# Performance work log

Hardware: AMD Instinct MI355X
Metric: run time of the kernel (lower is better)

Reference implementation:

```python
import jax, jax.numpy as jnp
import numpy as np
import math

HIDDEN = 2048
N_Q = 16
N_KV = 8
HEAD_DIM = 128
THETA = 10000.0
RANK = 8
ALPHA = 16
LORA_SCALING = ALPHA / RANK  # 2.0
SCALING = 1.0 / math.sqrt(HEAD_DIM)


def setup_inputs() -> dict:
    key = jax.random.key(0)
    ks = jax.random.split(key, 14)
    B, S = 2, 2048
    std = 0.02
    inp = {
        "x": jax.random.normal(ks[0], (B, S, HIDDEN), dtype=jnp.float32),
        # nn.Linear weights: [out_features, in_features]
        "Wq": jax.random.normal(ks[1], (N_Q * HEAD_DIM, HIDDEN), dtype=jnp.float32) * std,
        "Wk": jax.random.normal(ks[2], (N_KV * HEAD_DIM, HIDDEN), dtype=jnp.float32) * std,
        "Wv": jax.random.normal(ks[3], (N_KV * HEAD_DIM, HIDDEN), dtype=jnp.float32) * std,
        "Wo": jax.random.normal(ks[4], (HIDDEN, N_Q * HEAD_DIM), dtype=jnp.float32) * std,
        "qA": jax.random.normal(ks[5], (RANK, HIDDEN), dtype=jnp.float32) * std,
        "qB": jax.random.normal(ks[6], (N_Q * HEAD_DIM, RANK), dtype=jnp.float32) * std,
        "kA": jax.random.normal(ks[7], (RANK, HIDDEN), dtype=jnp.float32) * std,
        "kB": jax.random.normal(ks[8], (N_KV * HEAD_DIM, RANK), dtype=jnp.float32) * std,
        "vA": jax.random.normal(ks[9], (RANK, HIDDEN), dtype=jnp.float32) * std,
        "vB": jax.random.normal(ks[10], (N_KV * HEAD_DIM, RANK), dtype=jnp.float32) * std,
        "oA": jax.random.normal(ks[11], (RANK, N_Q * HEAD_DIM), dtype=jnp.float32) * std,
        "oB": jax.random.normal(ks[12], (HIDDEN, RANK), dtype=jnp.float32) * std,
    }
    return inp


def _rope_cos_sin(seq_len, dtype):
    inv_freq = 1.0 / (THETA ** (jnp.arange(0, HEAD_DIM, 2, dtype=jnp.float32) / HEAD_DIM))
    t = jnp.arange(seq_len, dtype=jnp.float32)
    freqs = t[:, None] * inv_freq[None, :]  # [S, D/2]
    return jnp.cos(freqs).astype(dtype), jnp.sin(freqs).astype(dtype)


def _apply_rope(x, cos, sin):
    # x: [B, H, S, D]; interleaved real/imag pairs on last dim
    xr = x[..., ::2]
    xi = x[..., 1::2]
    rr = xr * cos - xi * sin
    ri = xr * sin + xi * cos
    return jnp.stack([rr, ri], axis=-1).reshape(x.shape)


def _forward(x, Wq, Wk, Wv, Wo, qA, qB, kA, kB, vA, vB, oA, oB):
    B, S, H = x.shape
    # base projections + LoRA (low-rank path kept factored: (x @ A^T) @ B^T)
    q = x @ Wq.T + ((x @ qA.T) @ qB.T) * LORA_SCALING  # [B,S,NQ*D]
    k = x @ Wk.T + ((x @ kA.T) @ kB.T) * LORA_SCALING  # [B,S,NKV*D]
    v = x @ Wv.T + ((x @ vA.T) @ vB.T) * LORA_SCALING
    q = q.reshape(B, S, N_Q, HEAD_DIM).transpose(0, 2, 1, 3)   # [B,NQ,S,D]
    k = k.reshape(B, S, N_KV, HEAD_DIM).transpose(0, 2, 1, 3)  # [B,NKV,S,D]
    v = v.reshape(B, S, N_KV, HEAD_DIM).transpose(0, 2, 1, 3)
    cos, sin = _rope_cos_sin(S, x.dtype)  # [S, D/2] each
    q = _apply_rope(q, cos, sin)
    k = _apply_rope(k, cos, sin)
    if N_Q != N_KV:
        rep = N_Q // N_KV
        k = jnp.repeat(k, rep, axis=1)  # [B,NQ,S,D]
        v = jnp.repeat(v, rep, axis=1)
    scores = jnp.einsum('bhqd,bhkd->bhqk', q, k) * SCALING
    causal = jnp.tril(jnp.ones((S, S), dtype=bool))
    scores = jnp.where(causal, scores, -jnp.inf)
    attn = jax.nn.softmax(scores, axis=-1).astype(v.dtype)
    out = jnp.einsum('bhqk,bhkd->bhqd', attn, v)  # [B,NQ,S,D]
    out = out.transpose(0, 2, 1, 3).reshape(B, S, N_Q * HEAD_DIM)
    return out @ Wo.T + ((out @ oA.T) @ oB.T) * LORA_SCALING


def reference(x, Wq, Wk, Wv, Wo, qA, qB, kA, kB, vA, vB, oA, oB):
    return _forward(x, Wq, Wk, Wv, Wo, qA, qB, kA, kB, vA, vB, oA, oB)
```

## Files before the change

kernel.cpp:

```cpp
#include <hip/hip_runtime.h>
#include <hip/hip_bf16.h>
#include <cmath>

#define HIDDEN 2048
#define SEQ 2048
#define BATCH 2
#define NQ 16
#define NKV 8
#define HD 128
#define RANKL 8
#define LORA_SCALE 2.0f
#define INV_SQRT_D 0.08838834764831845f
#define LOG2E 1.4426950408889634f
#define SM_SCALE (INV_SQRT_D * LOG2E)

typedef unsigned short ushort_t;
typedef __bf16 bf16x8 __attribute__((ext_vector_type(8)));
typedef float f32x4 __attribute__((ext_vector_type(4)));

static __device__ __forceinline__ ushort_t f2bf(float f) {
    __hip_bfloat16 h = __float2bfloat16(f);
    return *(ushort_t*)&h;
}
static __device__ __forceinline__ float bf2f(ushort_t u) {
    unsigned int v = ((unsigned int)u) << 16;
    return __builtin_bit_cast(float, v);
}
static __device__ __forceinline__ void gload_lds16(const ushort_t* g, ushort_t* l) {
    __builtin_amdgcn_global_load_lds(
        (const __attribute__((address_space(1))) unsigned int*)g,
        (__attribute__((address_space(3))) unsigned int*)l, 16, 0, 0);
}
static __device__ __forceinline__ bf16x8 pack8(float4 a, float4 b) {
    uint4 u;
    u.x = (unsigned int)f2bf(a.x) | ((unsigned int)f2bf(a.y) << 16);
    u.y = (unsigned int)f2bf(a.z) | ((unsigned int)f2bf(a.w) << 16);
    u.z = (unsigned int)f2bf(b.x) | ((unsigned int)f2bf(b.y) << 16);
    u.w = (unsigned int)f2bf(b.z) | ((unsigned int)f2bf(b.w) << 16);
    return __builtin_bit_cast(bf16x8, u);
}

#define PREP_UNITS 10496
__global__ __launch_bounds__(256) void prep_fused(
    const float* __restrict__ X, ushort_t* __restrict__ Xbf,
    const float* __restrict__ qA, const float* __restrict__ kA,
    const float* __restrict__ vA,
    float* __restrict__ xa_q, float* __restrict__ xa_k,
    float* __restrict__ xa_v,
    const float* __restrict__ Wq, const float* __restrict__ Wk,
    const float* __restrict__ Wv, const float* __restrict__ Wo,
    ushort_t* __restrict__ Wqb, ushort_t* __restrict__ Wkb,
    ushort_t* __restrict__ Wvb, ushort_t* __restrict__ Wob)
{
    __shared__ f32x4 red[4][2][64];
    const int t = threadIdx.x;

    for (int bid = blockIdx.x; bid < PREP_UNITS; bid += gridDim.x) {
        if (bid < 4096) {
            int c0 = t * 8;
            const float* xr = X + (size_t)bid * HIDDEN + c0;
            float4 a = *(const float4*)xr;
            float4 b = *(const float4*)(xr + 4);
            uint4 o;
            o.x = (unsigned int)f2bf(a.x) | ((unsigned int)f2bf(a.y) << 16);
            o.y = (unsigned int)f2bf(a.z) | ((unsigned int)f2bf(a.w) << 16);
            o.z = (unsigned int)f2bf(b.x) | ((unsigned int)f2bf(b.y) << 16);
            o.w = (unsigned int)f2bf(b.z) | ((unsigned int)f2bf(b.w) << 16);
            *(uint4*)(Xbf + (size_t)bid * HIDDEN + c0) = o;
        } else if (bid < 10240) {
            size_t i = (size_t)(bid - 4096) * 256 + t;
            const float* src; ushort_t* dst; size_t j;
            if (i < 524288)       { src = Wq; dst = Wqb; j = i; }
            else if (i < 786432)  { src = Wk; dst = Wkb; j = i - 524288; }
            else if (i < 1048576) { src = Wv; dst = Wvb; j = i - 786432; }
            else                  { src = Wo; dst = Wob; j = i - 1048576; }
            const float4* p = (const float4*)src + j * 2;
            float4 a = p[0], b = p[1];
            uint4 o;
            o.x = (unsigned int)f2bf(a.x) | ((unsigned int)f2bf(a.y) << 16);
            o.y = (unsigned int)f2bf(a.z) | ((unsigned int)f2bf(a.w) << 16);
            o.z = (unsigned int)f2bf(b.x) | ((unsigned int)f2bf(b.y) << 16);
            o.w = (unsigned int)f2bf(b.z) | ((unsigned int)f2bf(b.w) << 16);
            *(uint4*)(dst + j * 8) = o;
        } else {
            const int m0 = (bid - 10240) * 16;
            const int lane = t & 63;
            const int w = t >> 6;
            const int c = lane & 15;
            const int quad = lane >> 4;

            const float* b0 = (c < 8) ? (qA + (size_t)c * HIDDEN)
                                      : (kA + (size_t)(c - 8) * HIDDEN);
            const float* b1 = vA + (size_t)(c & 7) * HIDDEN;
            const bool b1v = (c < 8);
            const float* ax = X + (size_t)(m0 + c) * HIDDEN;

            f32x4 acc0 = (f32x4){0.f, 0.f, 0.f, 0.f};
            f32x4 acc1 = (f32x4){0.f, 0.f, 0.f, 0.f};
            const int kbase = w * 512 + quad * 8;
#pragma unroll
            for (int ks = 0; ks < 16; ++ks) {
                const int k = kbase + ks * 32;
                float4 x0 = *(const float4*)&ax[k];
                float4 x1 = *(const float4*)&ax[k + 4];
                float4 p0a = *(const float4*)&b0[k];
                float4 p0b = *(const float4*)&b0[k + 4];
                float4 p1a = {0.f, 0.f, 0.f, 0.f}, p1b = {0.f, 0.f, 0.f, 0.f};
                if (b1v) { p1a = *(const float4*)&b1[k]; p1b = *(const float4*)&b1[k + 4]; }
                bf16x8 af = pack8(x0, x1);
                bf16x8 bf0 = pack8(p0a, p0b);
                bf16x8 bf1 = pack8(p1a, p1b);
                acc0 = __builtin_amdgcn_mfma_f32_16x16x32_bf16(af, bf0, acc0, 0, 0, 0);
                acc1 = __builtin_amdgcn_mfma_f32_16x16x32_bf16(af, bf1, acc1, 0, 0, 0);
            }
            red[w][0][lane] = acc0;
            red[w][1][lane] = acc1;
            __syncthreads();
            if (t < 64) {
#pragma unroll
                for (int nt = 0; nt < 2; ++nt) {
                    f32x4 s = red[0][nt][t];
#pragma unroll
                    for (int ww = 1; ww < 4; ++ww) {
                        f32x4 o = red[ww][nt][t];
                        s[0] += o[0]; s[1] += o[1]; s[2] += o[2]; s[3] += o[3];
                    }
                    int col = nt * 16 + (t & 15);
                    if (col < 24) {
                        float* dst = (col < 8) ? xa_q : (col < 16) ? xa_k : xa_v;
                        int cc = col & 7;
                        int row0 = m0 + (t >> 4) * 4;
#pragma unroll
                        for (int r = 0; r < 4; ++r)
                            dst[(size_t)(row0 + r) * RANKL + cc] = s[r];
                    }
                }
            }
            __syncthreads();
        }
    }
}

__global__ __launch_bounds__(256) void lora_o_mfma(
    const ushort_t* __restrict__ Xo, const float* __restrict__ oA,
    float* __restrict__ xa_o)
{
    __shared__ f32x4 red[4][64];
    const int t = threadIdx.x;
    const int lane = t & 63;
    const int w = t >> 6;
    const int c = lane & 15;
    const int quad = lane >> 4;
    const int m0 = blockIdx.x * 16;

    const ushort_t* ax = Xo + (size_t)(m0 + c) * (NQ * HD);
    const float* b0 = oA + (size_t)(c & 7) * (NQ * HD);
    const bool bv = (c < 8);

    f32x4 acc = (f32x4){0.f, 0.f, 0.f, 0.f};
    const int kbase = w * 512 + quad * 8;
#pragma unroll
    for (int ks = 0; ks < 16; ++ks) {
        const int k = kbase + ks * 32;
        bf16x8 af = *(const bf16x8*)&ax[k];
        float4 pa = {0.f, 0.f, 0.f, 0.f}, pb = {0.f, 0.f, 0.f, 0.f};
        if (bv) { pa = *(const float4*)&b0[k]; pb = *(const float4*)&b0[k + 4]; }
        bf16x8 bf = pack8(pa, pb);
        acc = __builtin_amdgcn_mfma_f32_16x16x32_bf16(af, bf, acc, 0, 0, 0);
    }
    red[w][lane] = acc;
    __syncthreads();
    if (t < 64) {
        f32x4 s = red[0][t];
#pragma unroll
        for (int ww = 1; ww < 4; ++ww) {
            f32x4 o = red[ww][t];
            s[0] += o[0]; s[1] += o[1]; s[2] += o[2]; s[3] += o[3];
        }
        int col = t & 15;
        if (col < 8) {
            int row0 = m0 + (t >> 4) * 4;
#pragma unroll
            for (int r = 0; r < 4; ++r)
                xa_o[(size_t)(row0 + r) * RANKL + col] = s[r];
        }
    }
}

static __device__ __forceinline__ void gemm_core(
    const ushort_t* __restrict__ A, const ushort_t* __restrict__ B,
    void* __restrict__ Cout, int N, int K, int bm, int bn,
    const float* __restrict__ xa, const float* __restrict__ LB,
    float lscale, int out_bf16, ushort_t* As, ushort_t* Bs)
{
    const int t = threadIdx.x;
    const int lane = t & 63;
    const int w = t >> 6;
    const int quad = lane >> 4;
    const int c = lane & 15;

    const int wm = (w & 1) * 64;
    const int wn = (w >> 1) * 64;

    f32x4 acc[4][4];
#pragma unroll
    for (int i = 0; i < 4; i++)
#pragma unroll
        for (int j = 0; j < 4; j++) acc[i][j] = (f32x4){0.f, 0.f, 0.f, 0.f};

    const int p0 = w * 64 + lane;
    const int p1 = 256 + w * 64 + lane;
    const int r0 = p0 >> 2, g0 = (p0 & 3) ^ ((p0 >> 3) & 3);
    const int r1 = p1 >> 2, g1 = (p1 & 3) ^ ((p1 >> 3) & 3);
    const ushort_t* gA0 = A + (size_t)(bm + r0) * K + g0 * 8;
    const ushort_t* gA1 = A + (size_t)(bm + r1) * K + g1 * 8;
    const ushort_t* gB0 = B + (size_t)(bn + r0) * K + g0 * 8;
    const ushort_t* gB1 = B + (size_t)(bn + r1) * K + g1 * 8;
    ushort_t* lA0 = As + (size_t)(w * 64) * 8;
    ushort_t* lA1 = As + (size_t)(256 + w * 64) * 8;
    ushort_t* lB0 = Bs + (size_t)(w * 64) * 8;
    ushort_t* lB1 = Bs + (size_t)(256 + w * 64) * 8;

    const int csw = quad ^ ((c >> 1) & 3);

    for (int k0 = 0; k0 < K; k0 += 32) {
        __syncthreads();
        gload_lds16(gA0 + k0, lA0);
        gload_lds16(gA1 + k0, lA1);
        gload_lds16(gB0 + k0, lB0);
        gload_lds16(gB1 + k0, lB1);
        __syncthreads();

        bf16x8 af[4], bfr[4];
#pragma unroll
        for (int mt = 0; mt < 4; mt++)
            af[mt] = *(const bf16x8*)&As[((wm + mt * 16 + c) * 4 + csw) * 8];
#pragma unroll
        for (int nt = 0; nt < 4; nt++)
            bfr[nt] = *(const bf16x8*)&Bs[((wn + nt * 16 + c) * 4 + csw) * 8];
#pragma unroll
        for (int mt = 0; mt < 4; mt++)
#pragma unroll
            for (int nt = 0; nt < 4; nt++)
                acc[mt][nt] = __builtin_amdgcn_mfma_f32_16x16x32_bf16(
                    af[mt], bfr[nt], acc[mt][nt], 0, 0, 0);
    }

    float lb[4][RANKL];
#pragma unroll
    for (int nt = 0; nt < 4; nt++) {
        int col = bn + wn + nt * 16 + c;
        float4 u = *(const float4*)&LB[(size_t)col * RANKL];
        float4 v = *(const float4*)&LB[(size_t)col * RANKL + 4];
        lb[nt][0] = u.x; lb[nt][1] = u.y; lb[nt][2] = u.z; lb[nt][3] = u.w;
        lb[nt][4] = v.x; lb[nt][5] = v.y; lb[nt][6] = v.z; lb[nt][7] = v.w;
    }
#pragma unroll
    for (int mt = 0; mt < 4; mt++) {
        float la[4][RANKL];
#pragma unroll
        for (int r = 0; r < 4; r++) {
            int row = bm + wm + mt * 16 + quad * 4 + r;
            float4 u = *(const float4*)&xa[(size_t)row * RANKL];
            float4 v = *(const float4*)&xa[(size_t)row * RANKL + 4];
            la[r][0] = u.x; la[r][1] = u.y; la[r][2] = u.z; la[r][3] = u.w;
            la[r][4] = v.x; la[r][5] = v.y; la[r][6] = v.z; la[r][7] = v.w;
        }
#pragma unroll
        for (int nt = 0; nt < 4; nt++) {
#pragma unroll
            for (int r = 0; r < 4; r++) {
                float s = 0.f;
#pragma unroll
                for (int k = 0; k < RANKL; k++) s += la[r][k] * lb[nt][k];
                float val = acc[mt][nt][r] + lscale * s;
                size_t row = bm + wm + mt * 16 + quad * 4 + r;
                size_t col = bn + wn + nt * 16 + c;
                if (out_bf16)
                    ((ushort_t*)Cout)[row * N + col] = f2bf(val);
                else
                    ((float*)Cout)[row * N + col] = val;
            }
        }
    }
}

#define BKT 64
#define NKT (HIDDEN / BKT)

__global__ __launch_bounds__(512, 2) void gemm_qkv256(
    const ushort_t* __restrict__ A,
    const ushort_t* __restrict__ Wqb, const ushort_t* __restrict__ Wkb,
    const ushort_t* __restrict__ Wvb,
    ushort_t* __restrict__ q_lin, ushort_t* __restrict__ k_lin,
    ushort_t* __restrict__ v_lin,
    const float* __restrict__ xa_q, const float* __restrict__ xa_k,
    const float* __restrict__ xa_v,
    const float* __restrict__ qB, const float* __restrict__ kB,
    const float* __restrict__ vB)
{
    __shared__ __align__(16) ushort_t As[2][256 * BKT];
    __shared__ __align__(16) ushort_t Bs[2][256 * BKT];

    const int t = threadIdx.x;
    const int lane = t & 63;
    const int w = t >> 6;
    const int wm = w >> 2;
    const int wn = w & 3;
    const int quad = lane >> 4;
    const int c = lane & 15;
    const int c7 = c & 7;

    const int bc = blockIdx.y;
    const ushort_t* Bmat; ushort_t* Cout; const float* xa; const float* LB;
    int N, bn;
    if (bc < 8)       { Bmat = Wqb; Cout = q_lin; xa = xa_q; LB = qB; N = 2048; bn = bc * 256; }
    else if (bc < 12) { Bmat = Wkb; Cout = k_lin; xa = xa_k; LB = kB; N = 1024; bn = (bc - 8) * 256; }
    else              { Bmat = Wvb; Cout = v_lin; xa = xa_v; LB = vB; N = 1024; bn = (bc - 12) * 256; }
    const int bm = blockIdx.x * 256;

    const int r8  = lane >> 3;
    const int ksl = (lane & 7) ^ r8;
    const int ga  = wn;
    const int bh  = wn >> 1;
    const int gb  = wm * 2 + (wn & 1);

    const ushort_t* gAb = A    + (size_t)(bm + wm * 128 + ga * 8 + r8) * HIDDEN + ksl * 8;
    const ushort_t* gBb = Bmat + (size_t)(bn + bh * 128 + gb * 8 + r8) * HIDDEN + ksl * 8;
    const int lAoff = (wm * 128 + ga * 8) * BKT;
    const int lBoff = (bh * 128 + gb * 8) * BKT;

#pragma unroll
    for (int j = 0; j < 4; j++) {
        gload_lds16(gAb + (size_t)j * 32 * HIDDEN, &As[0][lAoff + j * 32 * BKT]);
        gload_lds16(gBb + (size_t)j * 32 * HIDDEN, &Bs[0][lBoff + j * 32 * BKT]);
    }
#pragma unroll
    for (int j = 0; j < 3; j++) {
        gload_lds16(gAb + (size_t)j * 32 * HIDDEN + BKT, &As[1][lAoff + j * 32 * BKT]);
        gload_lds16(gBb + (size_t)j * 32 * HIDDEN + BKT, &Bs[1][lBoff + j * 32 * BKT]);
    }

    f32x4 acc[8][4];
#pragma unroll
    for (int i = 0; i < 8; i++)
#pragma unroll
        for (int j = 0; j < 4; j++) acc[i][j] = (f32x4){0.f, 0.f, 0.f, 0.f};

#pragma unroll 1
    for (int T = 0; T < NKT; ++T) {
        const int cur = T & 1;
        const ushort_t* cA = As[cur];
        const ushort_t* cB = Bs[cur];
        bf16x8 bfr[4][2];

#pragma unroll
        for (int q = 0; q < 4; ++q) {
            if (q == 0) {
                asm volatile("s_waitcnt vmcnt(6)" ::: "memory");
            }
            __builtin_amdgcn_sched_barrier(0);
            __builtin_amdgcn_s_barrier();
            __builtin_amdgcn_sched_barrier(0);

            bf16x8 af[2][2];
#pragma unroll
            for (int m2 = 0; m2 < 2; ++m2) {
                const int row = wm * 128 + (q * 2 + m2) * 16 + c;
#pragma unroll
                for (int kh = 0; kh < 2; ++kh)
                    af[m2][kh] = *(const bf16x8*)
                        &cA[row * BKT + (((kh * 4 + quad) ^ c7) * 8)];
            }
            if (q == 0) {
#pragma unroll
                for (int nt = 0; nt < 4; ++nt) {
                    const int rowb = wn * 64 + nt * 16 + c;
#pragma unroll
                    for (int kh = 0; kh < 2; ++kh)
                        bfr[nt][kh] = *(const bf16x8*)
                            &cB[rowb * BKT + (((kh * 4 + quad) ^ c7) * 8)];
                }
            }

            if (q == 0) {
                const int tl = T + 1;
                if (tl < NKT) {
                    gload_lds16(gAb + (size_t)3 * 32 * HIDDEN + (size_t)tl * BKT,
                                &As[cur ^ 1][lAoff + 3 * 32 * BKT]);
                    gload_lds16(gBb + (size_t)3 * 32 * HIDDEN + (size_t)tl * BKT,
                                &Bs[cur ^ 1][lBoff + 3 * 32 * BKT]);
                }
            } else {
                const int tl = T + 2;
                if (tl < NKT) {
                    const int j = q - 1;
                    gload_lds16(gAb + (size_t)j * 32 * HIDDEN + (size_t)tl * BKT,
                                &As[cur][lAoff + j * 32 * BKT]);
                    gload_lds16(gBb + (size_t)j * 32 * HIDDEN + (size_t)tl * BKT,
                                &Bs[cur][lBoff + j * 32 * BKT]);
                }
            }

            __builtin_amdgcn_s_setprio(1);
#pragma unroll
            for (int m2 = 0; m2 < 2; ++m2)
#pragma unroll
                for (int nt = 0; nt < 4; ++nt)
#pragma unroll
                    for (int kh = 0; kh < 2; ++kh)
                        acc[q * 2 + m2][nt] = __builtin_amdgcn_mfma_f32_16x16x32_bf16(
                            af[m2][kh], bfr[nt][kh], acc[q * 2 + m2][nt], 0, 0, 0);
            __builtin_amdgcn_s_setprio(0);
        }
    }

    float lb[4][RANKL];
#pragma unroll
    for (int nt = 0; nt < 4; nt++) {
        int col = bn + wn * 64 + nt * 16 + c;
        float4 u = *(const float4*)&LB[(size_t)col * RANKL];
        float4 v = *(const float4*)&LB[(size_t)col * RANKL + 4];
        lb[nt][0] = u.x; lb[nt][1] = u.y; lb[nt][2] = u.z; lb[nt][3] = u.w;
        lb[nt][4] = v.x; lb[nt][5] = v.y; lb[nt][6] = v.z; lb[nt][7] = v.w;
    }
#pragma unroll
    for (int mt = 0; mt < 8; mt++) {
        float la[4][RANKL];
#pragma unroll
        for (int r = 0; r < 4; r++) {
            int row = bm + wm * 128 + mt * 16 + quad * 4 + r;
            float4 u = *(const float4*)&xa[(size_t)row * RANKL];
            float4 v = *(const float4*)&xa[(size_t)row * RANKL + 4];
            la[r][0] = u.x; la[r][1] = u.y; la[r][2] = u.z; la[r][3] = u.w;
            la[r][4] = v.x; la[r][5] = v.y; la[r][6] = v.z; la[r][7] = v.w;
        }
#pragma unroll
        for (int nt = 0; nt < 4; nt++) {
#pragma unroll
            for (int r = 0; r < 4; r++) {
                float s = 0.f;
#pragma unroll
                for (int k = 0; k < RANKL; k++) s += la[r][k] * lb[nt][k];
                float val = acc[mt][nt][r] + LORA_SCALE * s;
                size_t row = bm + wm * 128 + mt * 16 + quad * 4 + r;
                size_t col = bn + wn * 64 + nt * 16 + c;
                Cout[row * N + col] = f2bf(val);
            }
        }
    }
}

__global__ __launch_bounds__(256) void gemm_wo(
    const ushort_t* __restrict__ A, const ushort_t* __restrict__ Wob,
    float* __restrict__ out, const float* __restrict__ xa_o,
    const float* __restrict__ oB)
{
    __shared__ ushort_t As[128 * 32];
    __shared__ ushort_t Bs[128 * 32];
    gemm_core(A, Wob, out, HIDDEN, NQ * HD, blockIdx.x * 128, blockIdx.y * 128,
              xa_o, oB, LORA_SCALE, 0, As, Bs);
}

#define RESHAPE_UNITS 5120
__global__ __launch_bounds__(256) void reshape_fused(
    const ushort_t* __restrict__ qlin, const ushort_t* __restrict__ klin,
    ushort_t* __restrict__ qb, ushort_t* __restrict__ kb,
    const ushort_t* __restrict__ vlin, ushort_t* __restrict__ Vt)
{
    __shared__ ushort_t tile[64 * 72];
    int t = threadIdx.x;
    for (int bid = blockIdx.x; bid < RESHAPE_UNITS; bid += gridDim.x) {
        if (bid < 4096) {
            int bs = bid;
            int s = bs & (SEQ - 1);
            int b = bs >> 11;
            int p = t & 63;
            float inv = exp2f(-(float)p * 0.20762050593046f);
            float ang = (float)s * inv;
            float cc = cosf(ang), si = sinf(ang);
#pragma unroll
            for (int j = 0; j < 6; j++) {
                int item = t + 256 * j;
                int hh = item >> 6;
                unsigned int pk;
                ushort_t* dst;
                if (hh < NQ) {
                    pk = *(const unsigned int*)&qlin[(size_t)bs * (NQ * HD) + hh * HD + 2 * p];
                    dst = qb + (((size_t)(b * NQ + hh) * SEQ) + s) * HD + 2 * p;
                } else {
                    int kh = hh - NQ;
                    pk = *(const unsigned int*)&klin[(size_t)bs * (NKV * HD) + kh * HD + 2 * p];
                    dst = kb + (((size_t)(b * NKV + kh) * SEQ) + s) * HD + 2 * p;
                }
                float xr = bf2f((ushort_t)(pk & 0xffff));
                float xi = bf2f((ushort_t)(pk >> 16));
                float rr = xr * cc - xi * si;
                float ri = xr * si + xi * cc;
                *(unsigned int*)dst = ((unsigned int)f2bf(ri) << 16) | f2bf(rr);
            }
        } else {
            int idx = bid - 4096;
            int bk = idx >> 6;
            int rem = idx & 63;
            int b = bk >> 3, kvh = bk & 7;
            int s0 = (rem >> 1) * 64, d0 = (rem & 1) * 64;
#pragma unroll
            for (int i = 0; i < 2; i++) {
                int id = t + 256 * i;
                int r = id >> 3, cc = id & 7;
                uint4 v = *(const uint4*)&vlin[(size_t)(b * SEQ + s0 + r) * (NKV * HD)
                                               + kvh * HD + d0 + cc * 8];
                *(uint4*)&tile[r * 72 + cc * 8] = v;
            }
            __syncthreads();
#pragma unroll
            for (int i = 0; i < 2; i++) {
                int id = t + 256 * i;
                int dr = id >> 3, sc = id & 7;
                ushort_t tmp[8];
#pragma unroll
                for (int e = 0; e < 8; e++) tmp[e] = tile[(sc * 8 + e) * 72 + dr];
                *(uint4*)&Vt[((size_t)(b * NKV + kvh) * HD + d0 + dr) * SEQ + s0 + sc * 8]
                    = *(uint4*)tmp;
            }
            __syncthreads();
        }
    }
}

__global__ __launch_bounds__(256, 2) void attn_mfma3(
    const ushort_t* __restrict__ Q, const ushort_t* __restrict__ K,
    const ushort_t* __restrict__ V, ushort_t* __restrict__ O)
{
    __shared__ ushort_t Ks[2][64 * 128];
    __shared__ ushort_t Vs[2][128 * 64];
    __shared__ ushort_t Psh[4][16 * 68];

    const int t = threadIdx.x;
    const int lane = t & 63;
    const int w = t >> 6;
    const int quad = lane >> 4;
    const int c = lane & 15;
    const int q4 = quad * 4;
    const int c7 = c & 7;

    const int head = blockIdx.x >> 4;
    const int a = blockIdx.x & 15;
    const int h = head & (NQ - 1);
    const int b = head >> 4;
    const int kvh = b * NKV + (h >> 1);

    const ushort_t* Kg = K + (size_t)kvh * SEQ * HD;
    const ushort_t* Vg = V + (size_t)kvh * HD * SEQ;

    const ushort_t* gK[4]; const ushort_t* gV[4];
    int lo[4];
#pragma unroll
    for (int i = 0; i < 4; i++) {
        int cid = t + 256 * i;
        int kr = cid >> 4, kc = cid & 15;
        gK[i] = Kg + (size_t)kr * HD + ((kc ^ (kr & 7)) * 8);
        int vd = cid >> 3, vc = cid & 7;
        gV[i] = Vg + (size_t)vd * SEQ + ((vc ^ (vd & 7)) * 8);
        lo[i] = (i * 256 + (t & ~63)) * 8;
    }

#pragma unroll 1
    for (int half = 0; half < 2; half++) {
        const int qt = half ? (31 - a) : a;
        const int qb0 = qt * 64;
        const int myrow = qb0 + w * 16;

        const ushort_t* Qg = Q + ((size_t)head * SEQ + myrow + c) * HD;
        bf16x8 qf[4];
#pragma unroll
        for (int ch = 0; ch < 4; ch++)
            qf[ch] = *(const bf16x8*)(Qg + ch * 32 + quad * 8);

        f32x4 o[8];
#pragma unroll
        for (int i = 0; i < 8; i++) o[i] = (f32x4){0.f, 0.f, 0.f, 0.f};
        float lp[4] = {0.f, 0.f, 0.f, 0.f};

        const int ntiles = qt + 1;

#pragma unroll
        for (int i = 0; i < 4; i++) gload_lds16(gK[i], &Ks[0][lo[i]]);
#pragma unroll
        for (int i = 0; i < 4; i++) gload_lds16(gV[i], &Vs[0][lo[i]]);
        __syncthreads();

        for (int tile = 0; tile < ntiles; ++tile) {
            const int cur = tile & 1;
            if (tile + 1 < ntiles) {
                const int j1 = (tile + 1) * 64;
#pragma unroll
                for (int i = 0; i < 4; i++)
                    gload_lds16(gK[i] + (size_t)j1 * HD, &Ks[cur ^ 1][lo[i]]);
#pragma unroll
                for (int i = 0; i < 4; i++)
                    gload_lds16(gV[i] + j1, &Vs[cur ^ 1][lo[i]]);
            }

            f32x4 s[4];
#pragma unroll
            for (int tt = 0; tt < 4; tt++) s[tt] = (f32x4){0.f, 0.f, 0.f, 0.f};
#pragma unroll
            for (int tt = 0; tt < 4; tt++) {
                const int krow = tt * 16 + c;
#pragma unroll
                for (int ch = 0; ch < 4; ch++) {
                    bf16x8 kf = *(const bf16x8*)
                        &Ks[cur][krow * 128 + (((ch * 4 + quad) ^ c7) * 8)];
                    s[tt] = __builtin_amdgcn_mfma_f32_16x16x32_bf16(
                        qf[ch], kf, s[tt], 0, 0, 0);
                }
            }

            const bool diag = (tile == qt);
            const int j0 = tile * 64;
#pragma unroll
            for (int r = 0; r < 4; r++) {
                const int row_g = myrow + q4 + r;
#pragma unroll
                for (int tt = 0; tt < 4; tt++) {
                    float p = exp2f(s[tt][r] * SM_SCALE);
                    if (diag && (j0 + tt * 16 + c > row_g)) p = 0.f;
                    Psh[w][(q4 + r) * 68 + tt * 16 + c] = f2bf(p);
                    lp[r] += p;
                }
            }

            bf16x8 pf[2];
#pragma unroll
            for (int ch = 0; ch < 2; ch++) {
                int base = c * 68 + ch * 32 + quad * 8;
                uint2 aa = *(const uint2*)&Psh[w][base];
                uint2 bb = *(const uint2*)&Psh[w][base + 4];
                uint4 u; u.x = aa.x; u.y = aa.y; u.z = bb.x; u.w = bb.y;
                pf[ch] = __builtin_bit_cast(bf16x8, u);
            }

#pragma unroll
            for (int dt = 0; dt < 8; dt++) {
                const int vrow = dt * 16 + c;
#pragma unroll
                for (int ch = 0; ch < 2; ch++) {
                    bf16x8 vf = *(const bf16x8*)
                        &Vs[cur][vrow * 64 + (((ch * 4 + quad) ^ c7) * 8)];
                    o[dt] = __builtin_amdgcn_mfma_f32_16x16x32_bf16(
                        pf[ch], vf, o[dt], 0, 0, 0);
                }
            }
            __syncthreads();
        }

        float inv[4];
#pragma unroll
        for (int r = 0; r < 4; r++) {
            float v = lp[r];
            v += __shfl_xor(v, 1);
            v += __shfl_xor(v, 2);
            v += __shfl_xor(v, 4);
            v += __shfl_xor(v, 8);
            inv[r] = 1.f / v;
        }
        size_t base = ((size_t)b * SEQ + myrow + q4) * (NQ * HD) + h * HD + c;
#pragma unroll
        for (int r = 0; r < 4; r++)
#pragma unroll
            for (int dt = 0; dt < 8; dt++)
                O[base + (size_t)r * (NQ * HD) + dt * 16] =
                    f2bf(o[dt][r] * inv[r]);
    }
}

extern "C" void kernel_launch(void* const* d_in, const int* in_sizes, int n_in,
                              void* d_out, int out_size, void* d_ws, size_t ws_size,
                              hipStream_t stream)
{
    const float* x  = (const float*)d_in[0];
    const float* Wq = (const float*)d_in[1];
    const float* Wk = (const float*)d_in[2];
    const float* Wv = (const float*)d_in[3];
    const float* Wo = (const float*)d_in[4];
    const float* qA = (const float*)d_in[5];
    const float* qB = (const float*)d_in[6];
    const float* kA = (const float*)d_in[7];
    const float* kB = (const float*)d_in[8];
    const float* vA = (const float*)d_in[9];
    const float* vB = (const float*)d_in[10];
    const float* oA = (const float*)d_in[11];
    const float* oB = (const float*)d_in[12];
    float* out = (float*)d_out;
    float* ws = (float*)d_ws;

    const int M = BATCH * SEQ;

    float* xa_q = ws;
    float* xa_k = ws + 32768;
    float* xa_v = ws + 65536;
    float* xa_o = ws + 98304;
    ushort_t* q_lin = (ushort_t*)(ws + 131072);
    ushort_t* k_lin = (ushort_t*)(ws + 4325376);
    ushort_t* v_lin = (ushort_t*)(ws + 6422528);
    ushort_t* qb    = (ushort_t*)(ws + 8519680);
    ushort_t* kb    = (ushort_t*)(ws + 12713984);
    ushort_t* vtb   = (ushort_t*)(ws + 14811136);
    ushort_t* xbf   = (ushort_t*)(ws + 16908288);
    ushort_t* Wqb   = (ushort_t*)(ws + 21102592);
    ushort_t* Wkb   = (ushort_t*)(ws + 23199744);
    ushort_t* Wvb   = (ushort_t*)(ws + 24248320);
    ushort_t* Wob   = (ushort_t*)(ws + 25296896);
    ushort_t* attn_out = q_lin;

    prep_fused<<<2048, 256, 0, stream>>>(
        x, xbf, qA, kA, vA, xa_q, xa_k, xa_v,
        Wq, Wk, Wv, Wo, Wqb, Wkb, Wvb, Wob);

    gemm_qkv256<<<dim3(M / 256, 16), 512, 0, stream>>>(
        xbf, Wqb, Wkb, Wvb, q_lin, k_lin, v_lin,
        xa_q, xa_k, xa_v, qB, kB, vB);

    reshape_fused<<<2048, 256, 0, stream>>>(
        q_lin, k_lin, qb, kb, v_lin, vtb);

    attn_mfma3<<<512, 256, 0, stream>>>(qb, kb, vtb, attn_out);

    lora_o_mfma<<<256, 256, 0, stream>>>(attn_out, oA, xa_o);
    gemm_wo<<<dim3(M / 128, HIDDEN / 128), 256, 0, stream>>>(
        attn_out, Wob, out, xa_o, oB);
}
```

Before: 346.3 us.

## Switch attention to 32x32 MFMA with 2x2 wave split over queries and keys

Rewrites the attention kernel so each wave computes a 32x32 score tile with 32x32x16 bf16 MFMAs, splitting the 64 key columns of each tile between wave pairs. Partial output accumulators and row sums from the two key-halves are combined through LDS at the end. The K LDS swizzle is widened to 16 chunks to match the new access pattern. The aim is fewer, larger MFMA instructions and better fragment reuse, at the cost of an extra LDS reduction and synchronization per query block.

```diff
diff --git a/kernel.cpp b/kernel.cpp
--- a/kernel.cpp
+++ b/kernel.cpp
@@ -17,6 +17,7 @@
 typedef unsigned short ushort_t;
 typedef __bf16 bf16x8 __attribute__((ext_vector_type(8)));
 typedef float f32x4 __attribute__((ext_vector_type(4)));
+typedef float f32x16 __attribute__((ext_vector_type(16)));
 
 static __device__ __forceinline__ ushort_t f2bf(float f) {
     __hip_bfloat16 h = __float2bfloat16(f);
@@ -529,21 +530,21 @@
     }
 }
 
-__global__ __launch_bounds__(256, 2) void attn_mfma3(
+__global__ __launch_bounds__(256, 2) void attn_mfma6(
     const ushort_t* __restrict__ Q, const ushort_t* __restrict__ K,
     const ushort_t* __restrict__ V, ushort_t* __restrict__ O)
 {
     __shared__ ushort_t Ks[2][64 * 128];
     __shared__ ushort_t Vs[2][128 * 64];
-    __shared__ ushort_t Psh[4][16 * 68];
+    __shared__ ushort_t Psh[4][32 * 36];
 
     const int t = threadIdx.x;
     const int lane = t & 63;
     const int w = t >> 6;
-    const int quad = lane >> 4;
-    const int c = lane & 15;
-    const int q4 = quad * 4;
-    const int c7 = c & 7;
+    const int qh = w >> 1;
+    const int kh = w & 1;
+    const int l31 = lane & 31;
+    const int hi = lane >> 5;
 
     const int head = blockIdx.x >> 4;
     const int a = blockIdx.x & 15;
@@ -560,7 +561,7 @@
     for (int i = 0; i < 4; i++) {
         int cid = t + 256 * i;
         int kr = cid >> 4, kc = cid & 15;
-        gK[i] = Kg + (size_t)kr * HD + ((kc ^ (kr & 7)) * 8);
+        gK[i] = Kg + (size_t)kr * HD + ((kc ^ (kr & 15)) * 8);
         int vd = cid >> 3, vc = cid & 7;
         gV[i] = Vg + (size_t)vd * SEQ + ((vc ^ (vd & 7)) * 8);
         lo[i] = (i * 256 + (t & ~63)) * 8;
@@ -570,18 +571,22 @@
     for (int half = 0; half < 2; half++) {
         const int qt = half ? (31 - a) : a;
         const int qb0 = qt * 64;
-        const int myrow = qb0 + w * 16;
-
-        const ushort_t* Qg = Q + ((size_t)head * SEQ + myrow + c) * HD;
-        bf16x8 qf[4];
-#pragma unroll
-        for (int ch = 0; ch < 4; ch++)
-            qf[ch] = *(const bf16x8*)(Qg + ch * 32 + quad * 8);
-
-        f32x4 o[8];
-#pragma unroll
-        for (int i = 0; i < 8; i++) o[i] = (f32x4){0.f, 0.f, 0.f, 0.f};
-        float lp[4] = {0.f, 0.f, 0.f, 0.f};
+        const int myq = qb0 + qh * 32;
+
+        const ushort_t* Qg = Q + ((size_t)head * SEQ + myq + l31) * HD;
+        bf16x8 qf[8];
+#pragma unroll
+        for (int kd = 0; kd < 8; kd++)
+            qf[kd] = *(const bf16x8*)(Qg + kd * 16 + hi * 8);
+
+        f32x16 o[4];
+#pragma unroll
+        for (int dt = 0; dt < 4; dt++)
+#pragma unroll
+            for (int i = 0; i < 16; i++) o[dt][i] = 0.f;
+        float lp[16];
+#pragma unroll
+        for (int i = 0; i < 16; i++) lp[i] = 0.f;
 
         const int ntiles = qt + 1;
 
@@ -603,76 +608,97 @@
                     gload_lds16(gV[i] + j1, &Vs[cur ^ 1][lo[i]]);
             }
 
-            f32x4 s[4];
-#pragma unroll
-            for (int tt = 0; tt < 4; tt++) s[tt] = (f32x4){0.f, 0.f, 0.f, 0.f};
-#pragma unroll
-            for (int tt = 0; tt < 4; tt++) {
-                const int krow = tt * 16 + c;
-#pragma unroll
-                for (int ch = 0; ch < 4; ch++) {
-                    bf16x8 kf = *(const bf16x8*)
-                        &Ks[cur][krow * 128 + (((ch * 4 + quad) ^ c7) * 8)];
-                    s[tt] = __builtin_amdgcn_mfma_f32_16x16x32_bf16(
-                        qf[ch], kf, s[tt], 0, 0, 0);
+            f32x16 s;
+#pragma unroll
+            for (int i = 0; i < 16; i++) s[i] = 0.f;
+            const int krow = kh * 32 + l31;
+#pragma unroll
+            for (int kd = 0; kd < 8; kd++) {
+                bf16x8 kf = *(const bf16x8*)
+                    &Ks[cur][krow * 128 + (((kd * 2 + hi) ^ (krow & 15)) * 8)];
+                s = __builtin_amdgcn_mfma_f32_32x32x16_bf16(qf[kd], kf, s, 0, 0, 0);
+            }
+
+            const bool diag = (tile == qt);
+            const int col_g = tile * 64 + kh * 32 + l31;
+#pragma unroll
+            for (int rg = 0; rg < 16; rg++) {
+                float p = exp2f(s[rg] * SM_SCALE);
+                const int R = (rg & 3) + 8 * (rg >> 2) + 4 * hi;
+                if (diag && (col_g > myq + R)) p = 0.f;
+                Psh[w][R * 36 + l31] = f2bf(p);
+                lp[rg] += p;
+            }
+
+            bf16x8 pf[2];
+#pragma unroll
+            for (int kc2 = 0; kc2 < 2; kc2++) {
+                int basep = l31 * 36 + kc2 * 16 + hi * 8;
+                uint2 aa = *(const uint2*)&Psh[w][basep];
+                uint2 bb = *(const uint2*)&Psh[w][basep + 4];
+                uint4 u; u.x = aa.x; u.y = aa.y; u.z = bb.x; u.w = bb.y;
+                pf[kc2] = __builtin_bit_cast(bf16x8, u);
+            }
+
+#pragma unroll
+            for (int dt = 0; dt < 4; dt++) {
+                const int d = dt * 32 + l31;
+#pragma unroll
+                for (int kc2 = 0; kc2 < 2; kc2++) {
+                    bf16x8 vf = *(const bf16x8*)
+                        &Vs[cur][d * 64 + (((kh * 4 + kc2 * 2 + hi) ^ (d & 7)) * 8)];
+                    o[dt] = __builtin_amdgcn_mfma_f32_32x32x16_bf16(
+                        pf[kc2], vf, o[dt], 0, 0, 0);
                 }
             }
-
-            const bool diag = (tile == qt);
-            const int j0 = tile * 64;
-#pragma unroll
-            for (int r = 0; r < 4; r++) {
-                const int row_g = myrow + q4 + r;
-#pragma unroll
-                for (int tt = 0; tt < 4; tt++) {
-                    float p = exp2f(s[tt][r] * SM_SCALE);
-                    if (diag && (j0 + tt * 16 + c > row_g)) p = 0.f;
-                    Psh[w][(q4 + r) * 68 + tt * 16 + c] = f2bf(p);
-                    lp[r] += p;
-                }
-            }
-
-            bf16x8 pf[2];
-#pragma unroll
-            for (int ch = 0; ch < 2; ch++) {
-                int base = c * 68 + ch * 32 + quad * 8;
-                uint2 aa = *(const uint2*)&Psh[w][base];
-                uint2 bb = *(const uint2*)&Psh[w][base + 4];
-                uint4 u; u.x = aa.x; u.y = aa.y; u.z = bb.x; u.w = bb.y;
-                pf[ch] = __builtin_bit_cast(bf16x8, u);
-            }
-
-#pragma unroll
-            for (int dt = 0; dt < 8; dt++) {
-                const int vrow = dt * 16 + c;
-#pragma unroll
-                for (int ch = 0; ch < 2; ch++) {
-                    bf16x8 vf = *(const bf16x8*)
-                        &Vs[cur][vrow * 64 + (((ch * 4 + quad) ^ c7) * 8)];
-                    o[dt] = __builtin_amdgcn_mfma_f32_16x16x32_bf16(
-                        pf[ch], vf, o[dt], 0, 0, 0);
-                }
-            }
             __syncthreads();
         }
 
-        float inv[4];
-#pragma unroll
-        for (int r = 0; r < 4; r++) {
-            float v = lp[r];
+#pragma unroll
+        for (int rg = 0; rg < 16; rg++) {
+            float v = lp[rg];
             v += __shfl_xor(v, 1);
             v += __shfl_xor(v, 2);
             v += __shfl_xor(v, 4);
             v += __shfl_xor(v, 8);
-            inv[r] = 1.f / v;
-        }
-        size_t base = ((size_t)b * SEQ + myrow + q4) * (NQ * HD) + h * HD + c;
-#pragma unroll
-        for (int r = 0; r < 4; r++)
-#pragma unroll
-            for (int dt = 0; dt < 8; dt++)
-                O[base + (size_t)r * (NQ * HD) + dt * 16] =
-                    f2bf(o[dt][r] * inv[r]);
+            v += __shfl_xor(v, 16);
+            lp[rg] = v;
+        }
+        float* osh  = qh ? (float*)&Vs[0][0] : (float*)&Ks[0][0];
+        float* lpsh = (float*)&Psh[0][0];
+        if (kh) {
+#pragma unroll
+            for (int dt = 0; dt < 4; dt++)
+#pragma unroll
+                for (int rg = 0; rg < 16; rg++)
+                    osh[lane * 65 + dt * 16 + rg] = o[dt][rg];
+            if (l31 == 0) {
+#pragma unroll
+                for (int rg = 0; rg < 16; rg++) {
+                    int R = (rg & 3) + 8 * (rg >> 2) + 4 * hi;
+                    lpsh[qh * 32 + R] = lp[rg];
+                }
+            }
+        }
+        __syncthreads();
+        if (!kh) {
+            float invv[16];
+#pragma unroll
+            for (int rg = 0; rg < 16; rg++) {
+                int R = (rg & 3) + 8 * (rg >> 2) + 4 * hi;
+                invv[rg] = 1.f / (lp[rg] + lpsh[qh * 32 + R]);
+            }
+            size_t rowbase = (size_t)b * SEQ + myq;
+#pragma unroll
+            for (int dt = 0; dt < 4; dt++)
+#pragma unroll
+                for (int rg = 0; rg < 16; rg++) {
+                    int R = (rg & 3) + 8 * (rg >> 2) + 4 * hi;
+                    float val = (o[dt][rg] + osh[lane * 65 + dt * 16 + rg]) * invv[rg];
+                    O[(rowbase + R) * (NQ * HD) + h * HD + dt * 32 + l31] = f2bf(val);
+                }
+        }
+        __syncthreads();
     }
 }
 
@@ -726,7 +752,7 @@
     reshape_fused<<<2048, 256, 0, stream>>>(
         q_lin, k_lin, qb, kb, v_lin, vtb);
 
-    attn_mfma3<<<512, 256, 0, stream>>>(qb, kb, vtb, attn_out);
+    attn_mfma6<<<512, 256, 0, stream>>>(qb, kb, vtb, attn_out);
 
     lora_o_mfma<<<256, 256, 0, stream>>>(attn_out, oA, xa_o);
     gemm_wo<<<dim3(M / 128, HIDDEN / 128), 256, 0, stream>>>(
```

Result: slower. 354.3 us (+2.3%).
